# Optimization experiments

Measured on AMD Instinct MI355X. Metric: run time of the kernel, lower is better.

The kernel has to match this reference:

```python
import jax, jax.numpy as jnp
import numpy as np

V, E, H, L, B, S = 32000, 512, 512, 2, 32, 128


def setup_inputs() -> dict:
    key = jax.random.key(0)
    ks = jax.random.split(key, 16)
    sc = 0.05
    return {
        "target": jax.random.randint(ks[0], (B, S), 0, V, dtype=jnp.int32),
        "target_length": jax.random.randint(ks[1], (B,), 1, S, dtype=jnp.int32),
        "context": jax.random.normal(ks[2], (L * 2, B, H), jnp.float32) * 0.1,
        "embed_table": jax.random.normal(ks[3], (V, E), jnp.float32) * sc,
        "w_ih0": jax.random.normal(ks[4], (2, 3 * H, E), jnp.float32) * sc,
        "w_hh0": jax.random.normal(ks[5], (2, 3 * H, H), jnp.float32) * sc,
        "b_ih0": jax.random.normal(ks[6], (2, 3 * H), jnp.float32) * sc,
        "b_hh0": jax.random.normal(ks[7], (2, 3 * H), jnp.float32) * sc,
        "w_ih1": jax.random.normal(ks[8], (2, 3 * H, 2 * H), jnp.float32) * sc,
        "w_hh1": jax.random.normal(ks[9], (2, 3 * H, H), jnp.float32) * sc,
        "b_ih1": jax.random.normal(ks[10], (2, 3 * H), jnp.float32) * sc,
        "b_hh1": jax.random.normal(ks[11], (2, 3 * H), jnp.float32) * sc,
        "fc_w": jax.random.normal(ks[12], (V, 2 * H), jnp.float32) * sc,
        "fc_b": jax.random.normal(ks[13], (V,), jnp.float32) * sc,
    }


def _gru_cell(x, h, w_ih, w_hh, b_ih, b_hh):
    # x: [B, in]  h: [2, B, H]  w_ih: [2, 3H, in]  w_hh: [2, 3H, H]
    gi = jnp.einsum('bi,dgi->dbg', x, w_ih) + b_ih[:, None, :]
    gh = jnp.einsum('dbh,dgh->dbg', h, w_hh) + b_hh[:, None, :]
    ir, iz, in_ = jnp.split(gi, 3, axis=-1)
    hr, hz, hn = jnp.split(gh, 3, axis=-1)
    r = jax.nn.sigmoid(ir + hr)
    z = jax.nn.sigmoid(iz + hz)
    n = jnp.tanh(in_ + r * hn)
    return (1.0 - z) * n + z * h  # [2, B, H]


def reference(target, target_length, context, embed_table,
              w_ih0, w_hh0, b_ih0, b_hh0,
              w_ih1, w_hh1, b_ih1, b_hh1,
              fc_w, fc_b):
    b, s = target.shape
    hd = context.shape[-1]
    emb = embed_table[target]                  # [B, S, E] (dropout = identity in eval)
    h0 = context.reshape(L, 2, b, hd)          # torch layout hidden[l*2+d]
    params = [(w_ih0, w_hh0, b_ih0, b_hh0), (w_ih1, w_hh1, b_ih1, b_hh1)]

    def step(h, x_t):                          # h: [L, 2, B, H], x_t: [B, E]
        x = x_t
        new_h = []
        for l in range(L):
            hn = _gru_cell(x, h[l], *params[l])            # [2, B, H]
            new_h.append(hn)
            x = hn.transpose(1, 0, 2).reshape(b, 2 * hd)   # concat fwd|bwd
        return jnp.stack(new_h), x

    _, outs = jax.lax.scan(step, h0, emb.transpose(1, 0, 2))  # outs: [S, B, 2H]
    out = outs.transpose(1, 0, 2)                              # [B, S, 2H]
    logits = jnp.einsum('bsh,vh->bsv', out, fc_w) + fc_b       # [B, S, V]
    return jax.nn.log_softmax(logits, axis=-1)
```

## Files before the change

### kernel.cpp

```cpp
#include <hip/hip_runtime.h>
#include <cstdint>
#include <cstddef>

#define Vv 32000
#define Ee 512
#define Hh 512
#define Bb 32
#define Ss 128

typedef __bf16 bf16x8 __attribute__((ext_vector_type(8)));
typedef float  f32x4  __attribute__((ext_vector_type(4)));
typedef unsigned long long ull;

__device__ __forceinline__ float b2f(unsigned short u) {
  union { unsigned int i; float f; } v; v.i = ((unsigned int)u) << 16; return v.f;
}
__device__ __forceinline__ unsigned short f2b(float f) {
  union { float f; unsigned int i; } v; v.f = f;
  unsigned int r = v.i + 0x7FFFu + ((v.i >> 16) & 1u);
  return (unsigned short)(r >> 16);
}
__device__ __forceinline__ float sigm(float x) { return 1.f / (1.f + __expf(-x)); }

__device__ __forceinline__ ull aload8(const unsigned short* p) {
  return __hip_atomic_load((const ull*)p, __ATOMIC_RELAXED, __HIP_MEMORY_SCOPE_AGENT);
}
__device__ __forceinline__ void astore8(unsigned short* p, ull v) {
  __hip_atomic_store((ull*)p, v, __ATOMIC_RELAXED, __HIP_MEMORY_SCOPE_AGENT);
}

__device__ __forceinline__ void gl_lds16(const unsigned short* g, unsigned short* l) {
  __builtin_amdgcn_global_load_lds(
      (const __attribute__((address_space(1))) void*)g,
      (__attribute__((address_space(3))) void*)l, 16, 0, 0);
}


__global__ void zero_flags(unsigned* p) {
  for (int i = threadIdx.x; i < 4096; i += 256) p[i] = 0u;
}

__global__ void cast_bf16(const float* __restrict__ src, unsigned short* __restrict__ dst, int n4) {
  int i = blockIdx.x * 256 + threadIdx.x;
  if (i >= n4) return;
  float4 v = reinterpret_cast<const float4*>(src)[i];
  ushort4 o;
  o.x = f2b(v.x); o.y = f2b(v.y); o.z = f2b(v.z); o.w = f2b(v.w);
  reinterpret_cast<ushort4*>(dst)[i] = o;
}

__global__ void pack_w1(const float* __restrict__ ih, const float* __restrict__ hh,
                        unsigned short* __restrict__ dst) {
  int r = blockIdx.x;
  const float* si = ih + (size_t)r * 1024;
  const float* sh = hh + (size_t)r * 512;
  unsigned short* dr = dst + (size_t)r * 1536;
  for (int c = threadIdx.x; c < 1024; c += 256) dr[c] = f2b(si[c]);
  for (int c = threadIdx.x; c < 512; c += 256) dr[1024 + c] = f2b(sh[c]);
}

__global__ void embed_gather(const int* __restrict__ target, const float* __restrict__ table,
                             unsigned short* __restrict__ emb) {
  int sb = blockIdx.x;
  int s = sb >> 5, b = sb & 31;
  int tok = target[b * Ss + s];
  float4 v = reinterpret_cast<const float4*>(table + (size_t)tok * Ee)[threadIdx.x];
  ushort4 o;
  o.x = f2b(v.x); o.y = f2b(v.y); o.z = f2b(v.z); o.w = f2b(v.w);
  reinterpret_cast<ushort4*>(emb + (size_t)sb * Ee)[threadIdx.x] = o;
}

template <int MODE>
__global__ __launch_bounds__(256, 2) void gemm_nt(
    const unsigned short* __restrict__ A, const unsigned short* __restrict__ Bm,
    const float* __restrict__ bias, void* __restrict__ Cout,
    int K, int ldc, size_t sBz, size_t sCz, size_t sBiasz,
    float* __restrict__ pm, float* __restrict__ ps) {
  int z = blockIdx.z;
  Bm += z * sBz;
  bias += z * sBiasz;

  __shared__ __align__(16) unsigned short As[128 * 64];
  __shared__ __align__(16) unsigned short Bs[128 * 64];
  __shared__ float smx[128][2], sse[128][2];

  int t = threadIdx.x;
  int bx, by;
  if (MODE == 1) {
    int lin = blockIdx.x + (int)gridDim.x * blockIdx.y;
    int q = (int)(gridDim.x * gridDim.y) >> 3;
    int wg = (lin & 7) * q + (lin >> 3);
    bx = wg & 31; by = wg >> 5;
  } else {
    bx = blockIdx.x; by = blockIdx.y;
  }
  int m0 = bx * 128, n0 = by * 128;
  int wave = t >> 6, lane = t & 63;
  int wr = wave >> 1, wc = wave & 1;

  f32x4 acc[4][4] = {};

  int kt = K >> 6;
  for (int ks = 0; ks < kt; ++ks) {
    int k0 = ks << 6;
#pragma unroll
    for (int c = 0; c < 4; ++c) {
      int v = c * 256 + t;
      int row = v >> 3, col = (v & 7) * 8;
      int vb = (c * 256 + (t & 192)) * 8;
      gl_lds16(A + (size_t)(m0 + row) * K + k0 + col, As + vb);
      gl_lds16(Bm + (size_t)(n0 + row) * K + k0 + col, Bs + vb);
    }
    __syncthreads();
#pragma unroll
    for (int kk = 0; kk < 2; ++kk) {
      bf16x8 af[4], bfr[4];
      int lrow = lane & 15, lk = kk * 32 + (lane >> 4) * 8;
#pragma unroll
      for (int m = 0; m < 4; ++m)
        af[m] = *reinterpret_cast<const bf16x8*>(As + (wr * 64 + m * 16 + lrow) * 64 + lk);
#pragma unroll
      for (int n = 0; n < 4; ++n)
        bfr[n] = *reinterpret_cast<const bf16x8*>(Bs + (wc * 64 + n * 16 + lrow) * 64 + lk);
#pragma unroll
      for (int m = 0; m < 4; ++m)
#pragma unroll
        for (int n = 0; n < 4; ++n)
          acc[m][n] = __builtin_amdgcn_mfma_f32_16x16x32_bf16(af[m], bfr[n], acc[m][n], 0, 0, 0);
    }
    __syncthreads();
  }

  int lrow4 = (lane >> 4) * 4, lcol = lane & 15;
  if (MODE == 0) {
#pragma unroll
    for (int m = 0; m < 4; ++m) {
      int rbase = m0 + wr * 64 + m * 16 + lrow4;
#pragma unroll
      for (int n = 0; n < 4; ++n) {
        int col = n0 + wc * 64 + n * 16 + lcol;
        float bv = bias[col];
#pragma unroll
        for (int j = 0; j < 4; ++j) {
          int r = rbase + j;
          float vv = acc[m][n][j] + bv;
          ((unsigned short*)Cout)[z * sCz + (size_t)r * ldc + col] = f2b(vv);
        }
      }
    }
  } else {
    float bv[4];
#pragma unroll
    for (int n = 0; n < 4; ++n) bv[n] = bias[n0 + wc * 64 + n * 16 + lcol];
#pragma unroll
    for (int m = 0; m < 4; ++m) {
#pragma unroll
      for (int j = 0; j < 4; ++j) {
        float x[4];
#pragma unroll
        for (int n = 0; n < 4; ++n) x[n] = acc[m][n][j] + bv[n];
        int rib = wr * 64 + m * 16 + lrow4 + j;
        int r = m0 + rib;
        int b = r & 31, s = r >> 5;
        float* crow = (float*)Cout + (size_t)(b * Ss + s) * ldc;
#pragma unroll
        for (int n = 0; n < 4; ++n)
          __builtin_nontemporal_store(x[n], crow + n0 + wc * 64 + n * 16 + lcol);
        float mx = fmaxf(fmaxf(x[0], x[1]), fmaxf(x[2], x[3]));
#pragma unroll
        for (int msk = 1; msk < 16; msk <<= 1) mx = fmaxf(mx, __shfl_xor(mx, msk, 16));
        float se = __expf(x[0] - mx) + __expf(x[1] - mx) + __expf(x[2] - mx) + __expf(x[3] - mx);
#pragma unroll
        for (int msk = 1; msk < 16; msk <<= 1) se += __shfl_xor(se, msk, 16);
        if (lcol == 0) { smx[rib][wc] = mx; sse[rib][wc] = se; }
      }
    }
    __syncthreads();
    if (t < 128) {
      float ma = smx[t][0], mb = smx[t][1];
      float M = fmaxf(ma, mb);
      float S = sse[t][0] * __expf(ma - M) + sse[t][1] * __expf(mb - M);
      int rg = m0 + t;
      int b = rg & 31, s = rg >> 5;
      size_t orow = (size_t)(b * Ss + s);
      pm[orow * 250 + by] = M;
      ps[orow * 250 + by] = S;
    }
  }
}


#define MFMA16 __builtin_amdgcn_mfma_f32_16x16x32_bf16
#define L1_STRIDE 1544
#define L0_STRIDE 520

__global__ __launch_bounds__(384, 1) void pers_kernel(
    const unsigned short* __restrict__ gi0,
    const unsigned short* __restrict__ whh0b, const unsigned short* __restrict__ w1cat,
    const float* __restrict__ b_hh0, const float* __restrict__ b_ih1, const float* __restrict__ b_hh1,
    const float* __restrict__ context,
    unsigned short* __restrict__ XH, unsigned short* __restrict__ H0,
    unsigned short* __restrict__ outs, unsigned* bar) {
  extern __shared__ __align__(16) unsigned short A_lds[];
  __shared__ float pre[7][16][33];
  __shared__ float hf[32][16];
  __shared__ float bA[16], bB[16], bC[16], bD[16];
  __shared__ unsigned sAbort;

  unsigned* flags = bar;
  unsigned* abortf = bar + 3072;

  const int tid = threadIdx.x, blk = blockIdx.x;
  const int w = tid >> 6, lane = tid & 63, ln = lane & 15;
  const int hi8 = (lane >> 4) * 8;
  const bool isL1 = blk < 64;
  const int d = (blk & 63) >> 5, j0 = (blk & 31) * 16;
  const int g = w >> 1, kh = w & 1;

  if (tid == 0) sAbort = 0u;

  auto stile = [&](int s, f32x4 v0, f32x4 v1) {
    int c = ln, r0 = (lane >> 4) * 4;
#pragma unroll
    for (int j = 0; j < 4; ++j) {
      pre[s][c][r0 + j] = v0[j];
      pre[s][c][16 + r0 + j] = v1[j];
    }
  };

  bf16x8 wreg[24];
  if (isL1) {
    const unsigned short* Bw =
        w1cat + ((size_t)d * 1536 + g * 512 + j0 + ln) * 1536 + kh * 768 + hi8;
#pragma unroll
    for (int i = 0; i < 24; ++i) wreg[i] = *reinterpret_cast<const bf16x8*>(Bw + i * 32);
  } else {
    const unsigned short* Bw =
        whh0b + ((size_t)d * 1536 + g * 512 + j0 + ln) * 512 + kh * 256 + hi8;
#pragma unroll
    for (int i = 0; i < 8; ++i) wreg[i] = *reinterpret_cast<const bf16x8*>(Bw + i * 32);
  }

  if (tid < 16) {
    int jj = tid;
    if (isL1) {
      bA[jj] = b_ih1[d * 1536 + j0 + jj] + b_hh1[d * 1536 + j0 + jj];
      bB[jj] = b_ih1[d * 1536 + 512 + j0 + jj] + b_hh1[d * 1536 + 512 + j0 + jj];
      bC[jj] = b_ih1[d * 1536 + 1024 + j0 + jj];
      bD[jj] = b_hh1[d * 1536 + 1024 + j0 + jj];
    } else {
      bA[jj] = b_hh0[d * 1536 + j0 + jj];
      bB[jj] = b_hh0[d * 1536 + 512 + j0 + jj];
      bC[jj] = b_hh0[d * 1536 + 1024 + j0 + jj];
    }
  }
  {
    int layer = isL1 ? 1 : 0;
    for (int i = tid; i < 128; i += 384) {
      int b = i >> 2, j4 = (i & 3) * 4;
      ull pk = 0;
#pragma unroll
      for (int k = 0; k < 4; ++k) {
        float c = context[(((size_t)layer * 2 + d) * 32 + b) * 512 + j0 + j4 + k];
        hf[b][j4 + k] = c;
        pk |= ((ull)f2b(c)) << (16 * k);
      }
      if (isL1) astore8(XH + (size_t)b * 2048 + 1024 + d * 512 + j0 + j4, pk);
      else      astore8(H0 + (size_t)3 * 32768 + ((size_t)d * 32 + b) * 512 + j0 + j4, pk);
    }
  }
  __syncthreads();
  if (tid == 0)
    __hip_atomic_store(flags + (size_t)blk * 16, 1u, __ATOMIC_RELAXED, __HIP_MEMORY_SCOPE_AGENT);

  for (int p = 0; p <= 128; ++p) {
    ull gr = 0, gz2 = 0, gn2 = 0;
    if (!isL1 && p <= 127 && tid < 128) {
      const unsigned short* gzp =
          gi0 + ((size_t)d * 128 + p) * 32 * 1536 + (size_t)(tid >> 2) * 1536 + j0 + (tid & 3) * 4;
      gr  = *(const ull*)(gzp);
      gz2 = *(const ull*)(gzp + 512);
      gn2 = *(const ull*)(gzp + 1024);
    }

    if (w < 2) {
      int idx = -1, tgt = 0;
      if (isL1) {
        if (w == 0) { if (lane < 64) { idx = 64 + lane; tgt = p + 1; } }
        else        { if (lane < 32) { idx = d * 32 + lane; tgt = p + 1; } }
      } else {
        if (w == 0) { if (lane < 32) { idx = 64 + d * 32 + lane; tgt = p + 1; } }
        else        { if (lane < 64) { idx = lane; tgt = p - 1; } }
      }
      ull t0 = __builtin_amdgcn_s_memrealtime();
      while (true) {
        int f = (idx >= 0)
            ? (int)__hip_atomic_load(flags + (size_t)idx * 16, __ATOMIC_RELAXED, __HIP_MEMORY_SCOPE_AGENT)
            : 0x7FFFFFF;
        if (__all(f >= tgt)) break;
        if ((__builtin_amdgcn_s_memrealtime() - t0) > 100000000ULL ||
            __hip_atomic_load(abortf, __ATOMIC_RELAXED, __HIP_MEMORY_SCOPE_AGENT) != 0u) {
          __hip_atomic_store(abortf, 1u, __ATOMIC_RELAXED, __HIP_MEMORY_SCOPE_AGENT);
          sAbort = 1u;
          break;
        }
        __builtin_amdgcn_s_sleep(1);
      }
    }
    __syncthreads();
    if (sAbort) return;

    int rs = (p - 1) & 3, wslot = p & 3;

    if (isL1) {
      if (p >= 1) {
        const unsigned short* XHp = XH + (size_t)rs * 65536;
        int col = tid * 4;
        int gcol = (col < 1024) ? col : (1024 + d * 512 + (col - 1024));
        const unsigned short* src = XHp + gcol;
        unsigned short* dstl = A_lds + col;
        ull v[32];
#pragma unroll
        for (int b = 0; b < 32; ++b) v[b] = aload8(src + (size_t)b * 2048);
#pragma unroll
        for (int b = 0; b < 32; ++b) *(ull*)(dstl + b * L1_STRIDE) = v[b];
      }
    } else {
      if (p <= 127) {
        const unsigned short* H0p = H0 + (size_t)rs * 32768 + (size_t)d * 32 * 512;
        ull v[11];
#pragma unroll
        for (int k = 0; k < 11; ++k) {
          int idx = tid + k * 384;
          if (idx < 4096) v[k] = aload8(H0p + (size_t)(idx >> 7) * 512 + (idx & 127) * 4);
        }
#pragma unroll
        for (int k = 0; k < 11; ++k) {
          int idx = tid + k * 384;
          if (idx < 4096) *(ull*)(A_lds + (idx >> 7) * L0_STRIDE + (idx & 127) * 4) = v[k];
        }
      }
    }
    __syncthreads();

    if (isL1) {
      if (p >= 1) {
        f32x4 p0 = {}, p1 = {}, q0 = {}, q1 = {};
        const unsigned short* al = A_lds + kh * 768 + hi8;
        if (g == 2 && kh == 1) {
#pragma unroll
          for (int i = 0; i < 8; ++i) {
            bf16x8 a0 = *reinterpret_cast<const bf16x8*>(al + ln * L1_STRIDE + i * 32);
            bf16x8 a1 = *reinterpret_cast<const bf16x8*>(al + (ln + 16) * L1_STRIDE + i * 32);
            p0 = MFMA16(a0, wreg[i], p0, 0, 0, 0);
            p1 = MFMA16(a1, wreg[i], p1, 0, 0, 0);
          }
#pragma unroll
          for (int i = 8; i < 24; ++i) {
            bf16x8 a0 = *reinterpret_cast<const bf16x8*>(al + ln * L1_STRIDE + i * 32);
            bf16x8 a1 = *reinterpret_cast<const bf16x8*>(al + (ln + 16) * L1_STRIDE + i * 32);
            q0 = MFMA16(a0, wreg[i], q0, 0, 0, 0);
            q1 = MFMA16(a1, wreg[i], q1, 0, 0, 0);
          }
          stile(5, p0, p1);
          stile(6, q0, q1);
        } else {
#pragma unroll
          for (int i = 0; i < 24; ++i) {
            bf16x8 a0 = *reinterpret_cast<const bf16x8*>(al + ln * L1_STRIDE + i * 32);
            bf16x8 a1 = *reinterpret_cast<const bf16x8*>(al + (ln + 16) * L1_STRIDE + i * 32);
            p0 = MFMA16(a0, wreg[i], p0, 0, 0, 0);
            p1 = MFMA16(a1, wreg[i], p1, 0, 0, 0);
          }
          stile((g < 2) ? g * 2 + kh : 4, p0, p1);
        }
      }
    } else {
      if (p <= 127) {
        f32x4 p0 = {}, p1 = {};
        const unsigned short* al = A_lds + kh * 256 + hi8;
#pragma unroll
        for (int i = 0; i < 8; ++i) {
          bf16x8 a0 = *reinterpret_cast<const bf16x8*>(al + ln * L0_STRIDE + i * 32);
          bf16x8 a1 = *reinterpret_cast<const bf16x8*>(al + (ln + 16) * L0_STRIDE + i * 32);
          p0 = MFMA16(a0, wreg[i], p0, 0, 0, 0);
          p1 = MFMA16(a1, wreg[i], p1, 0, 0, 0);
        }
        stile((g < 2) ? g * 2 + kh : 4 + kh, p0, p1);
      }
    }
    __syncthreads();

    if (isL1) {
      if (p >= 1 && tid < 128) {
        int t_ = p - 1;
        int b = tid >> 2, j4 = (tid & 3) * 4;
        ull pk = 0;
#pragma unroll
        for (int k = 0; k < 4; ++k) {
          int jj = j4 + k;
          float r = sigm(pre[0][jj][b] + pre[1][jj][b] + bA[jj]);
          float z = sigm(pre[2][jj][b] + pre[3][jj][b] + bB[jj]);
          float nn = tanhf(pre[4][jj][b] + pre[5][jj][b] + bC[jj] +
                           r * (pre[6][jj][b] + bD[jj]));
          float h = hf[b][jj];
          float hnew = (1.f - z) * nn + z * h;
          hf[b][jj] = hnew;
          pk |= ((ull)f2b(hnew)) << (16 * k);
        }
        astore8(XH + (size_t)wslot * 65536 + (size_t)b * 2048 + 1024 + d * 512 + j0 + j4, pk);
        __builtin_nontemporal_store(
            pk, (ull*)(outs + ((size_t)t_ * 32 + b) * 1024 + (size_t)d * 512 + j0 + j4));
      }
    } else {
      if (p <= 127 && tid < 128) {
        int b = tid >> 2, j4 = (tid & 3) * 4;
        int col = j0 + j4;
        ull pk = 0;
#pragma unroll
        for (int k = 0; k < 4; ++k) {
          int jj = j4 + k;
          float gir = b2f((unsigned short)(gr >> (16 * k)));
          float giz = b2f((unsigned short)(gz2 >> (16 * k)));
          float gin = b2f((unsigned short)(gn2 >> (16 * k)));
          float r = sigm(gir + pre[0][jj][b] + pre[1][jj][b] + bA[jj]);
          float z = sigm(giz + pre[2][jj][b] + pre[3][jj][b] + bB[jj]);
          float nn = tanhf(gin + r * (pre[4][jj][b] + pre[5][jj][b] + bC[jj]));
          float h = hf[b][jj];
          float hnew = (1.f - z) * nn + z * h;
          hf[b][jj] = hnew;
          pk |= ((ull)f2b(hnew)) << (16 * k);
        }
        astore8(H0 + (size_t)wslot * 32768 + ((size_t)d * 32 + b) * 512 + col, pk);
        astore8(XH + (size_t)wslot * 65536 + (size_t)b * 2048 + d * 512 + col, pk);
      }
    }
    __syncthreads();
    if (tid == 0)
      __hip_atomic_store(flags + (size_t)blk * 16, (unsigned)(p + 2),
                         __ATOMIC_RELAXED, __HIP_MEMORY_SCOPE_AGENT);
    if (!isL1 && p == 127) return;
  }
}


__global__ __launch_bounds__(128) void lse_reduce(const float* __restrict__ pm,
                                                  const float* __restrict__ ps,
                                                  float* __restrict__ lsebuf) {
  int r = blockIdx.x * 128 + threadIdx.x;
  const float* pmr = pm + (size_t)r * 250;
  const float* psr = ps + (size_t)r * 250;
  float M = -1e30f, S = 0.f;
  for (int i = 0; i < 250; ++i) {
    float m2 = pmr[i], s2 = psr[i];
    if (m2 <= M) {
      S += s2 * __expf(m2 - M);
    } else {
      S = S * __expf(M - m2) + s2;
      M = m2;
    }
  }
  lsebuf[r] = M + __logf(S);
}

__global__ __launch_bounds__(256) void sub_lse(float* __restrict__ out,
                                               const float* __restrict__ lsebuf) {
  int row = blockIdx.x;
  float l = lsebuf[row];
  f32x4* rp = (f32x4*)(out + (size_t)row * Vv);
  for (int i = threadIdx.x; i < 8000; i += 256) {
    f32x4 v = __builtin_nontemporal_load(rp + i);
    v[0] -= l; v[1] -= l; v[2] -= l; v[3] -= l;
    __builtin_nontemporal_store(v, rp + i);
  }
}


extern "C" void kernel_launch(void* const* d_in, const int* in_sizes, int n_in,
                              void* d_out, int out_size, void* d_ws, size_t ws_size,
                              hipStream_t stream) {
  (void)in_sizes; (void)n_in; (void)out_size; (void)ws_size;
  const int*   target  = (const int*)  d_in[0];
  const float* context = (const float*)d_in[2];
  const float* table   = (const float*)d_in[3];
  const float* w_ih0   = (const float*)d_in[4];
  const float* w_hh0   = (const float*)d_in[5];
  const float* b_ih0   = (const float*)d_in[6];
  const float* b_hh0   = (const float*)d_in[7];
  const float* w_ih1   = (const float*)d_in[8];
  const float* w_hh1   = (const float*)d_in[9];
  const float* b_ih1   = (const float*)d_in[10];
  const float* b_hh1   = (const float*)d_in[11];
  const float* fc_w    = (const float*)d_in[12];
  const float* fc_b    = (const float*)d_in[13];
  float* out = (float*)d_out;

  uint8_t* ws = (uint8_t*)d_ws;
  size_t off = 0;
  auto alloc = [&](size_t bytes) {
    uint8_t* p = ws + off;
    off += (bytes + 255) & ~(size_t)255;
    return p;
  };
  unsigned*       bar   = (unsigned*)alloc(16384);
  unsigned short* XH    = (unsigned short*)alloc((size_t)4 * 32 * 2048 * 2);
  unsigned short* H0    = (unsigned short*)alloc((size_t)4 * 2 * 32 * 512 * 2);
  unsigned short* whh0b = (unsigned short*)alloc((size_t)1572864 * 2);
  unsigned short* w1cat = (unsigned short*)alloc((size_t)2 * 1536 * 1536 * 2);
  unsigned short* embb  = (unsigned short*)alloc((size_t)2097152 * 2);
  unsigned short* wih0b = (unsigned short*)alloc((size_t)1572864 * 2);
  unsigned short* gi0   = (unsigned short*)alloc((size_t)12582912 * 2);
  unsigned short* outsb = (unsigned short*)alloc((size_t)4194304 * 2);
  unsigned short* fcwb  = (unsigned short*)alloc((size_t)32768000 * 2);

  float* pm     = (float*)gi0;
  float* ps     = pm + (size_t)4096 * 250;
  float* lsebuf = ps + (size_t)4096 * 250;

  static bool attr_done = false;
  if (!attr_done) {
    hipFuncSetAttribute(reinterpret_cast<const void*>(pers_kernel),
                        hipFuncAttributeMaxDynamicSharedMemorySize, 98816);
    attr_done = true;
  }

  zero_flags<<<dim3(1), 256, 0, stream>>>(bar);
  cast_bf16<<<dim3(1536), 256, 0, stream>>>(w_ih0, wih0b, 393216);
  cast_bf16<<<dim3(1536), 256, 0, stream>>>(w_hh0, whh0b, 393216);
  cast_bf16<<<dim3(32000), 256, 0, stream>>>(fc_w, fcwb, 8192000);
  pack_w1<<<dim3(3072), 256, 0, stream>>>(w_ih1, w_hh1, w1cat);
  embed_gather<<<dim3(4096), 128, 0, stream>>>(target, table, embb);

  gemm_nt<0><<<dim3(32, 12, 2), 256, 0, stream>>>(
      embb, wih0b, b_ih0, gi0, 512, 1536,
      (size_t)1536 * 512, (size_t)4096 * 1536, (size_t)1536, nullptr, nullptr);

  pers_kernel<<<dim3(128), 384, 98816, stream>>>(
      gi0, whh0b, w1cat, b_hh0, b_ih1, b_hh1, context, XH, H0, outsb, bar);

  gemm_nt<1><<<dim3(32, 250, 1), 256, 0, stream>>>(
      outsb, fcwb, fc_b, out, 1024, Vv, 0, 0, 0, pm, ps);

  lse_reduce<<<dim3(32), 128, 0, stream>>>(pm, ps, lsebuf);
  sub_lse<<<dim3(4096), 256, 0, stream>>>(out, lsebuf);
}
```

Baseline: 1.356 ms.

## Tag recurrent state with step numbers and overlap fc_w cast with persistent GRU

The persistent GRU kernel now publishes hidden states as 32-bit words that carry a step tag next to each bf16 value. Consumers poll the data itself instead of waiting on per-step flag barriers, the ring buffer grows to 8 slots, and the full flag wait runs only every 4 steps. The fc_w fp32-to-bf16 cast moves into 128 extra blocks of the persistent launch so it runs alongside the serial recurrence, and the small prep kernels are merged into one launch. This cuts per-step synchronisation latency and launch overhead, but doubles the bytes exchanged per step and risks the cast blocks competing with the recurrent blocks for memory bandwidth.

```diff
diff --git a/kernel.cpp b/kernel.cpp
--- a/kernel.cpp
+++ b/kernel.cpp
@@ -22,11 +22,19 @@
 }
 __device__ __forceinline__ float sigm(float x) { return 1.f / (1.f + __expf(-x)); }
 
-__device__ __forceinline__ ull aload8(const unsigned short* p) {
-  return __hip_atomic_load((const ull*)p, __ATOMIC_RELAXED, __HIP_MEMORY_SCOPE_AGENT);
-}
-__device__ __forceinline__ void astore8(unsigned short* p, ull v) {
-  __hip_atomic_store((ull*)p, v, __ATOMIC_RELAXED, __HIP_MEMORY_SCOPE_AGENT);
+__device__ __forceinline__ ull aload8(const ull* p) {
+  return __hip_atomic_load(p, __ATOMIC_RELAXED, __HIP_MEMORY_SCOPE_AGENT);
+}
+__device__ __forceinline__ void astore8(ull* p, ull v) {
+  __hip_atomic_store(p, v, __ATOMIC_RELAXED, __HIP_MEMORY_SCOPE_AGENT);
+}
+__device__ __forceinline__ unsigned pack32(ull v) {
+  return (unsigned)(v & 0xFFFFull) | (unsigned)((v >> 16) & 0xFFFF0000ull);
+}
+__device__ __forceinline__ ull packpair(float a, float b, unsigned tag) {
+  ull lo = (ull)((unsigned)f2b(a) | (tag << 16));
+  ull hi = (ull)((unsigned)f2b(b) | (tag << 16));
+  return lo | (hi << 32);
 }
 
 __device__ __forceinline__ void gl_lds16(const unsigned short* g, unsigned short* l) {
@@ -35,39 +43,42 @@
       (__attribute__((address_space(3))) void*)l, 16, 0, 0);
 }
 
-
-__global__ void zero_flags(unsigned* p) {
-  for (int i = threadIdx.x; i < 4096; i += 256) p[i] = 0u;
-}
-
-__global__ void cast_bf16(const float* __restrict__ src, unsigned short* __restrict__ dst, int n4) {
-  int i = blockIdx.x * 256 + threadIdx.x;
-  if (i >= n4) return;
-  float4 v = reinterpret_cast<const float4*>(src)[i];
-  ushort4 o;
-  o.x = f2b(v.x); o.y = f2b(v.y); o.z = f2b(v.z); o.w = f2b(v.w);
-  reinterpret_cast<ushort4*>(dst)[i] = o;
-}
-
-__global__ void pack_w1(const float* __restrict__ ih, const float* __restrict__ hh,
-                        unsigned short* __restrict__ dst) {
-  int r = blockIdx.x;
-  const float* si = ih + (size_t)r * 1024;
-  const float* sh = hh + (size_t)r * 512;
-  unsigned short* dr = dst + (size_t)r * 1536;
-  for (int c = threadIdx.x; c < 1024; c += 256) dr[c] = f2b(si[c]);
-  for (int c = threadIdx.x; c < 512; c += 256) dr[1024 + c] = f2b(sh[c]);
-}
-
-__global__ void embed_gather(const int* __restrict__ target, const float* __restrict__ table,
-                             unsigned short* __restrict__ emb) {
-  int sb = blockIdx.x;
-  int s = sb >> 5, b = sb & 31;
-  int tok = target[b * Ss + s];
-  float4 v = reinterpret_cast<const float4*>(table + (size_t)tok * Ee)[threadIdx.x];
-  ushort4 o;
-  o.x = f2b(v.x); o.y = f2b(v.y); o.z = f2b(v.z); o.w = f2b(v.w);
-  reinterpret_cast<ushort4*>(emb + (size_t)sb * Ee)[threadIdx.x] = o;
+__global__ __launch_bounds__(256) void prep_all(
+    const float* __restrict__ w_ih0, const float* __restrict__ w_hh0,
+    const float* __restrict__ w_ih1, const float* __restrict__ w_hh1,
+    const int* __restrict__ target, const float* __restrict__ table,
+    unsigned short* __restrict__ wih0b, unsigned short* __restrict__ whh0b,
+    unsigned short* __restrict__ w1cat, unsigned short* __restrict__ emb,
+    unsigned* __restrict__ bar) {
+  int blk = blockIdx.x, t = threadIdx.x;
+  if (blk < 1536) {
+    int i = blk * 256 + t;
+    float4 v = reinterpret_cast<const float4*>(w_ih0)[i];
+    ushort4 o; o.x = f2b(v.x); o.y = f2b(v.y); o.z = f2b(v.z); o.w = f2b(v.w);
+    reinterpret_cast<ushort4*>(wih0b)[i] = o;
+  } else if (blk < 3072) {
+    int i = (blk - 1536) * 256 + t;
+    float4 v = reinterpret_cast<const float4*>(w_hh0)[i];
+    ushort4 o; o.x = f2b(v.x); o.y = f2b(v.y); o.z = f2b(v.z); o.w = f2b(v.w);
+    reinterpret_cast<ushort4*>(whh0b)[i] = o;
+  } else if (blk < 6144) {
+    int r = blk - 3072;
+    const float* si = w_ih1 + (size_t)r * 1024;
+    const float* sh = w_hh1 + (size_t)r * 512;
+    unsigned short* dr = w1cat + (size_t)r * 1536;
+    for (int c = t; c < 1024; c += 256) dr[c] = f2b(si[c]);
+    for (int c = t; c < 512; c += 256) dr[1024 + c] = f2b(sh[c]);
+  } else if (blk < 8192) {
+    int sb = (blk - 6144) * 2 + (t >> 7);
+    int tt = t & 127;
+    int s = sb >> 5, b = sb & 31;
+    int tok = target[b * Ss + s];
+    float4 v = reinterpret_cast<const float4*>(table + (size_t)tok * Ee)[tt];
+    ushort4 o; o.x = f2b(v.x); o.y = f2b(v.y); o.z = f2b(v.z); o.w = f2b(v.w);
+    reinterpret_cast<ushort4*>(emb + (size_t)sb * Ee)[tt] = o;
+  } else {
+    for (int i = t; i < 4096; i += 256) bar[i] = 0u;
+  }
 }
 
 template <int MODE>
@@ -193,14 +204,29 @@
 #define MFMA16 __builtin_amdgcn_mfma_f32_16x16x32_bf16
 #define L1_STRIDE 1544
 #define L0_STRIDE 520
-
-__global__ __launch_bounds__(384, 1) void pers_kernel(
+#define TAGMASK 0xFFFF0000FFFF0000ull
+
+__global__ __launch_bounds__(512, 1) void pers_kernel(
     const unsigned short* __restrict__ gi0,
     const unsigned short* __restrict__ whh0b, const unsigned short* __restrict__ w1cat,
     const float* __restrict__ b_hh0, const float* __restrict__ b_ih1, const float* __restrict__ b_hh1,
     const float* __restrict__ context,
-    unsigned short* __restrict__ XH, unsigned short* __restrict__ H0,
-    unsigned short* __restrict__ outs, unsigned* bar) {
+    unsigned* __restrict__ XO, unsigned* __restrict__ H1,
+    unsigned short* __restrict__ outs, unsigned* bar,
+    const float* __restrict__ fc_w, unsigned short* __restrict__ fcwb) {
+  const int tid = threadIdx.x, blk = blockIdx.x;
+
+  if (blk >= 128) {
+    int base = (blk - 128) * 512 + tid;
+#pragma unroll 5
+    for (int i = base; i < 8192000; i += 65536) {
+      float4 v = reinterpret_cast<const float4*>(fc_w)[i];
+      ushort4 o; o.x = f2b(v.x); o.y = f2b(v.y); o.z = f2b(v.z); o.w = f2b(v.w);
+      reinterpret_cast<ushort4*>(fcwb)[i] = o;
+    }
+    return;
+  }
+
   extern __shared__ __align__(16) unsigned short A_lds[];
   __shared__ float pre[7][16][33];
   __shared__ float hf[32][16];
@@ -210,7 +236,6 @@
   unsigned* flags = bar;
   unsigned* abortf = bar + 3072;
 
-  const int tid = threadIdx.x, blk = blockIdx.x;
   const int w = tid >> 6, lane = tid & 63, ln = lane & 15;
   const int hi8 = (lane >> 4) * 8;
   const bool isL1 = blk < 64;
@@ -219,6 +244,23 @@
 
   if (tid == 0) sAbort = 0u;
 
+  auto pollwait = [&](int idx, unsigned tgt) {
+    ull t0 = __builtin_amdgcn_s_memrealtime();
+    while (true) {
+      unsigned f = (idx >= 0)
+          ? __hip_atomic_load(flags + (size_t)idx * 16, __ATOMIC_RELAXED, __HIP_MEMORY_SCOPE_AGENT)
+          : 0xFFFFFFFu;
+      if (__all(f >= tgt)) break;
+      if ((__builtin_amdgcn_s_memrealtime() - t0) > 100000000ULL ||
+          __hip_atomic_load(abortf, __ATOMIC_RELAXED, __HIP_MEMORY_SCOPE_AGENT) != 0u) {
+        __hip_atomic_store(abortf, 1u, __ATOMIC_RELAXED, __HIP_MEMORY_SCOPE_AGENT);
+        sAbort = 1u;
+        break;
+      }
+      __builtin_amdgcn_s_sleep(1);
+    }
+  };
+
   auto stile = [&](int s, f32x4 v0, f32x4 v1) {
     int c = ln, r0 = (lane >> 4) * 4;
 #pragma unroll
@@ -229,16 +271,18 @@
   };
 
   bf16x8 wreg[24];
-  if (isL1) {
-    const unsigned short* Bw =
-        w1cat + ((size_t)d * 1536 + g * 512 + j0 + ln) * 1536 + kh * 768 + hi8;
-#pragma unroll
-    for (int i = 0; i < 24; ++i) wreg[i] = *reinterpret_cast<const bf16x8*>(Bw + i * 32);
-  } else {
-    const unsigned short* Bw =
-        whh0b + ((size_t)d * 1536 + g * 512 + j0 + ln) * 512 + kh * 256 + hi8;
-#pragma unroll
-    for (int i = 0; i < 8; ++i) wreg[i] = *reinterpret_cast<const bf16x8*>(Bw + i * 32);
+  if (w < 6) {
+    if (isL1) {
+      const unsigned short* Bw =
+          w1cat + ((size_t)d * 1536 + g * 512 + j0 + ln) * 1536 + kh * 768 + hi8;
+#pragma unroll
+      for (int i = 0; i < 24; ++i) wreg[i] = *reinterpret_cast<const bf16x8*>(Bw + i * 32);
+    } else {
+      const unsigned short* Bw =
+          whh0b + ((size_t)d * 1536 + g * 512 + j0 + ln) * 512 + kh * 256 + hi8;
+#pragma unroll
+      for (int i = 0; i < 8; ++i) wreg[i] = *reinterpret_cast<const bf16x8*>(Bw + i * 32);
+    }
   }
 
   if (tid < 16) {
@@ -254,148 +298,214 @@
       bC[jj] = b_hh0[d * 1536 + 1024 + j0 + jj];
     }
   }
-  {
+
+  if (tid < 128) {
+    int b = tid >> 2, j4 = (tid & 3) * 4;
     int layer = isL1 ? 1 : 0;
-    for (int i = tid; i < 128; i += 384) {
-      int b = i >> 2, j4 = (i & 3) * 4;
-      ull pk = 0;
-#pragma unroll
-      for (int k = 0; k < 4; ++k) {
-        float c = context[(((size_t)layer * 2 + d) * 32 + b) * 512 + j0 + j4 + k];
-        hf[b][j4 + k] = c;
-        pk |= ((ull)f2b(c)) << (16 * k);
-      }
-      if (isL1) astore8(XH + (size_t)b * 2048 + 1024 + d * 512 + j0 + j4, pk);
-      else      astore8(H0 + (size_t)3 * 32768 + ((size_t)d * 32 + b) * 512 + j0 + j4, pk);
+    float c0 = context[(((size_t)layer * 2 + d) * 32 + b) * 512 + j0 + j4 + 0];
+    float c1 = context[(((size_t)layer * 2 + d) * 32 + b) * 512 + j0 + j4 + 1];
+    float c2 = context[(((size_t)layer * 2 + d) * 32 + b) * 512 + j0 + j4 + 2];
+    float c3 = context[(((size_t)layer * 2 + d) * 32 + b) * 512 + j0 + j4 + 3];
+    hf[b][j4 + 0] = c0; hf[b][j4 + 1] = c1; hf[b][j4 + 2] = c2; hf[b][j4 + 3] = c3;
+    if (isL1) {
+      ull* dst = (ull*)H1 + ((size_t)(0 * 2 + d) * 32 + b) * 256 + ((j0 + j4) >> 1);
+      astore8(dst, packpair(c0, c1, 1u));
+      astore8(dst + 1, packpair(c2, c3, 1u));
+    } else {
+      ull* dst = (ull*)XO + ((size_t)(7 * 32 + b)) * 512 + d * 256 + ((j0 + j4) >> 1);
+      astore8(dst, packpair(c0, c1, 0u));
+      astore8(dst + 1, packpair(c2, c3, 0u));
+    }
+#pragma unroll
+    for (int s = 0; s < 8; ++s) {
+      if (isL1 ? (s == 0) : (s == 7)) continue;
+      ull* dst = isL1
+          ? (ull*)H1 + (((size_t)s * 2 + d) * 32 + b) * 256 + ((j0 + j4) >> 1)
+          : (ull*)XO + ((size_t)s * 32 + b) * 512 + d * 256 + ((j0 + j4) >> 1);
+      astore8(dst, ~0ull);
+      astore8(dst + 1, ~0ull);
     }
   }
   __syncthreads();
   if (tid == 0)
     __hip_atomic_store(flags + (size_t)blk * 16, 1u, __ATOMIC_RELAXED, __HIP_MEMORY_SCOPE_AGENT);
-
-  for (int p = 0; p <= 128; ++p) {
-    ull gr = 0, gz2 = 0, gn2 = 0;
-    if (!isL1 && p <= 127 && tid < 128) {
-      const unsigned short* gzp =
-          gi0 + ((size_t)d * 128 + p) * 32 * 1536 + (size_t)(tid >> 2) * 1536 + j0 + (tid & 3) * 4;
-      gr  = *(const ull*)(gzp);
-      gz2 = *(const ull*)(gzp + 512);
-      gn2 = *(const ull*)(gzp + 1024);
-    }
-
-    if (w < 2) {
-      int idx = -1, tgt = 0;
-      if (isL1) {
-        if (w == 0) { if (lane < 64) { idx = 64 + lane; tgt = p + 1; } }
-        else        { if (lane < 32) { idx = d * 32 + lane; tgt = p + 1; } }
-      } else {
-        if (w == 0) { if (lane < 32) { idx = 64 + d * 32 + lane; tgt = p + 1; } }
-        else        { if (lane < 64) { idx = lane; tgt = p - 1; } }
-      }
-      ull t0 = __builtin_amdgcn_s_memrealtime();
-      while (true) {
-        int f = (idx >= 0)
-            ? (int)__hip_atomic_load(flags + (size_t)idx * 16, __ATOMIC_RELAXED, __HIP_MEMORY_SCOPE_AGENT)
-            : 0x7FFFFFF;
-        if (__all(f >= tgt)) break;
-        if ((__builtin_amdgcn_s_memrealtime() - t0) > 100000000ULL ||
-            __hip_atomic_load(abortf, __ATOMIC_RELAXED, __HIP_MEMORY_SCOPE_AGENT) != 0u) {
-          __hip_atomic_store(abortf, 1u, __ATOMIC_RELAXED, __HIP_MEMORY_SCOPE_AGENT);
-          sAbort = 1u;
-          break;
-        }
-        __builtin_amdgcn_s_sleep(1);
-      }
-    }
-    __syncthreads();
-    if (sAbort) return;
-
-    int rs = (p - 1) & 3, wslot = p & 3;
-
-    if (isL1) {
-      if (p >= 1) {
-        const unsigned short* XHp = XH + (size_t)rs * 65536;
-        int col = tid * 4;
-        int gcol = (col < 1024) ? col : (1024 + d * 512 + (col - 1024));
-        const unsigned short* src = XHp + gcol;
-        unsigned short* dstl = A_lds + col;
-        ull v[32];
-#pragma unroll
-        for (int b = 0; b < 32; ++b) v[b] = aload8(src + (size_t)b * 2048);
-#pragma unroll
-        for (int b = 0; b < 32; ++b) *(ull*)(dstl + b * L1_STRIDE) = v[b];
-      }
-    } else {
-      if (p <= 127) {
-        const unsigned short* H0p = H0 + (size_t)rs * 32768 + (size_t)d * 32 * 512;
-        ull v[11];
-#pragma unroll
-        for (int k = 0; k < 11; ++k) {
-          int idx = tid + k * 384;
-          if (idx < 4096) v[k] = aload8(H0p + (size_t)(idx >> 7) * 512 + (idx & 127) * 4);
-        }
-#pragma unroll
-        for (int k = 0; k < 11; ++k) {
-          int idx = tid + k * 384;
-          if (idx < 4096) *(ull*)(A_lds + (idx >> 7) * L0_STRIDE + (idx & 127) * 4) = v[k];
-        }
-      }
-    }
-    __syncthreads();
-
-    if (isL1) {
-      if (p >= 1) {
-        f32x4 p0 = {}, p1 = {}, q0 = {}, q1 = {};
-        const unsigned short* al = A_lds + kh * 768 + hi8;
-        if (g == 2 && kh == 1) {
+  if (w == 6) pollwait(lane, 1u);
+  else if (w == 7) pollwait(64 + lane, 1u);
+  __syncthreads();
+  bool dead = (sAbort != 0u);
+
+  if (!dead) {
+    for (int p = 0; p <= 128; ++p) {
+      bool l0act = (!isL1) && p <= 127;
+      bool l1act = isL1 && p >= 1;
+      int s_rd = (p - 1) & 7, s_wr = p & 7;
+      ull ex = ((ull)(unsigned)p << 16) | ((ull)(unsigned)p << 48);
+
+      ull gr = 0, gz2 = 0, gn2 = 0;
+      if (l0act && tid < 128) {
+        const unsigned short* gzp =
+            gi0 + ((size_t)d * 128 + p) * 32 * 1536 + (size_t)(tid >> 2) * 1536 + j0 + (tid & 3) * 4;
+        gr  = *(const ull*)(gzp);
+        gz2 = *(const ull*)(gzp + 512);
+        gn2 = *(const ull*)(gzp + 1024);
+      }
+
+      if ((p & 3) == 0 && p >= 4) {
+        if (isL1) {
+          if (w == 6) pollwait(lane < 32 ? d * 32 + lane : -1, (unsigned)(p - 2));
+        } else if (p <= 127) {
+          if (w == 6) pollwait(lane, (unsigned)(p - 2));
+          else if (w == 7) pollwait(lane < 32 ? 64 + d * 32 + lane : -1, (unsigned)(p - 2));
+        }
+      }
+
+      if (l1act) {
+        const ull* xw = (const ull*)XO + (size_t)s_rd * 16384;
+        const ull* hw = (const ull*)H1 + ((size_t)s_rd * 2 + d) * 8192;
+        ull vx[32], vh[16];
+#pragma unroll
+        for (int k = 0; k < 32; ++k) vx[k] = aload8(xw + tid + k * 512);
+#pragma unroll
+        for (int k = 0; k < 16; ++k) vh[k] = aload8(hw + tid + k * 512);
+        unsigned pendA = 0, pendB = 0;
+#pragma unroll
+        for (int k = 0; k < 32; ++k) {
+          int idx = tid + k * 512, b = idx >> 9, c2 = idx & 511;
+          if (((vx[k] ^ ex) & TAGMASK) == 0)
+            *(unsigned*)(A_lds + (size_t)b * L1_STRIDE + 2 * c2) = pack32(vx[k]);
+          else pendA |= 1u << k;
+        }
+#pragma unroll
+        for (int k = 0; k < 16; ++k) {
+          int idx = tid + k * 512, b = idx >> 8, c2 = idx & 255;
+          if (((vh[k] ^ ex) & TAGMASK) == 0)
+            *(unsigned*)(A_lds + (size_t)b * L1_STRIDE + 1024 + 2 * c2) = pack32(vh[k]);
+          else pendB |= 1u << k;
+        }
+        if (pendA | pendB) {
+          ull t0 = __builtin_amdgcn_s_memrealtime();
+          while (pendA | pendB) {
+#pragma unroll
+            for (int k = 0; k < 32; ++k) if ((pendA >> k) & 1) {
+              ull v = aload8(xw + tid + k * 512);
+              if (((v ^ ex) & TAGMASK) == 0) {
+                int idx = tid + k * 512, b = idx >> 9, c2 = idx & 511;
+                *(unsigned*)(A_lds + (size_t)b * L1_STRIDE + 2 * c2) = pack32(v);
+                pendA &= ~(1u << k);
+              }
+            }
+#pragma unroll
+            for (int k = 0; k < 16; ++k) if ((pendB >> k) & 1) {
+              ull v = aload8(hw + tid + k * 512);
+              if (((v ^ ex) & TAGMASK) == 0) {
+                int idx = tid + k * 512, b = idx >> 8, c2 = idx & 255;
+                *(unsigned*)(A_lds + (size_t)b * L1_STRIDE + 1024 + 2 * c2) = pack32(v);
+                pendB &= ~(1u << k);
+              }
+            }
+            if ((__builtin_amdgcn_s_memrealtime() - t0) > 100000000ULL ||
+                __hip_atomic_load(abortf, __ATOMIC_RELAXED, __HIP_MEMORY_SCOPE_AGENT) != 0u) {
+              __hip_atomic_store(abortf, 1u, __ATOMIC_RELAXED, __HIP_MEMORY_SCOPE_AGENT);
+              sAbort = 1u;
+              break;
+            }
+          }
+        }
+      } else if (l0act) {
+        const ull* xw = (const ull*)XO + (size_t)s_rd * 16384 + d * 256;
+        ull vx[16];
+#pragma unroll
+        for (int k = 0; k < 16; ++k) {
+          int idx = tid + k * 512;
+          vx[k] = aload8(xw + ((size_t)(idx >> 8) << 9) + (idx & 255));
+        }
+        unsigned pendA = 0;
+#pragma unroll
+        for (int k = 0; k < 16; ++k) {
+          int idx = tid + k * 512, b = idx >> 8, c2 = idx & 255;
+          if (((vx[k] ^ ex) & TAGMASK) == 0)
+            *(unsigned*)(A_lds + (size_t)b * L0_STRIDE + 2 * c2) = pack32(vx[k]);
+          else pendA |= 1u << k;
+        }
+        if (pendA) {
+          ull t0 = __builtin_amdgcn_s_memrealtime();
+          while (pendA) {
+#pragma unroll
+            for (int k = 0; k < 16; ++k) if ((pendA >> k) & 1) {
+              int idx = tid + k * 512;
+              ull v = aload8(xw + ((size_t)(idx >> 8) << 9) + (idx & 255));
+              if (((v ^ ex) & TAGMASK) == 0) {
+                int b = idx >> 8, c2 = idx & 255;
+                *(unsigned*)(A_lds + (size_t)b * L0_STRIDE + 2 * c2) = pack32(v);
+                pendA &= ~(1u << k);
+              }
+            }
+            if ((__builtin_amdgcn_s_memrealtime() - t0) > 100000000ULL ||
+                __hip_atomic_load(abortf, __ATOMIC_RELAXED, __HIP_MEMORY_SCOPE_AGENT) != 0u) {
+              __hip_atomic_store(abortf, 1u, __ATOMIC_RELAXED, __HIP_MEMORY_SCOPE_AGENT);
+              sAbort = 1u;
+              break;
+            }
+          }
+        }
+      }
+      __syncthreads();
+      if (sAbort) { dead = true; break; }
+      if (tid == 0 && (l1act || l0act))
+        __hip_atomic_store(flags + (size_t)blk * 16, (unsigned)(p + 2),
+                           __ATOMIC_RELAXED, __HIP_MEMORY_SCOPE_AGENT);
+
+      if (w < 6) {
+        if (l1act) {
+          f32x4 p0 = {}, p1 = {}, q0 = {}, q1 = {};
+          const unsigned short* al = A_lds + kh * 768 + hi8;
+          if (g == 2 && kh == 1) {
+#pragma unroll
+            for (int i = 0; i < 8; ++i) {
+              bf16x8 a0 = *reinterpret_cast<const bf16x8*>(al + ln * L1_STRIDE + i * 32);
+              bf16x8 a1 = *reinterpret_cast<const bf16x8*>(al + (ln + 16) * L1_STRIDE + i * 32);
+              p0 = MFMA16(a0, wreg[i], p0, 0, 0, 0);
+              p1 = MFMA16(a1, wreg[i], p1, 0, 0, 0);
+            }
+#pragma unroll
+            for (int i = 8; i < 24; ++i) {
+              bf16x8 a0 = *reinterpret_cast<const bf16x8*>(al + ln * L1_STRIDE + i * 32);
+              bf16x8 a1 = *reinterpret_cast<const bf16x8*>(al + (ln + 16) * L1_STRIDE + i * 32);
+              q0 = MFMA16(a0, wreg[i], q0, 0, 0, 0);
+              q1 = MFMA16(a1, wreg[i], q1, 0, 0, 0);
+            }
+            stile(5, p0, p1);
+            stile(6, q0, q1);
+          } else {
+#pragma unroll
+            for (int i = 0; i < 24; ++i) {
+              bf16x8 a0 = *reinterpret_cast<const bf16x8*>(al + ln * L1_STRIDE + i * 32);
+              bf16x8 a1 = *reinterpret_cast<const bf16x8*>(al + (ln + 16) * L1_STRIDE + i * 32);
+              p0 = MFMA16(a0, wreg[i], p0, 0, 0, 0);
+              p1 = MFMA16(a1, wreg[i], p1, 0, 0, 0);
+            }
+            stile((g < 2) ? g * 2 + kh : 4, p0, p1);
+          }
+        } else if (l0act) {
+          f32x4 p0 = {}, p1 = {};
+          const unsigned short* al = A_lds + kh * 256 + hi8;
 #pragma unroll
           for (int i = 0; i < 8; ++i) {
-            bf16x8 a0 = *reinterpret_cast<const bf16x8*>(al + ln * L1_STRIDE + i * 32);
-            bf16x8 a1 = *reinterpret_cast<const bf16x8*>(al + (ln + 16) * L1_STRIDE + i * 32);
+            bf16x8 a0 = *reinterpret_cast<const bf16x8*>(al + ln * L0_STRIDE + i * 32);
+            bf16x8 a1 = *reinterpret_cast<const bf16x8*>(al + (ln + 16) * L0_STRIDE + i * 32);
             p0 = MFMA16(a0, wreg[i], p0, 0, 0, 0);
             p1 = MFMA16(a1, wreg[i], p1, 0, 0, 0);
           }
-#pragma unroll
-          for (int i = 8; i < 24; ++i) {
-            bf16x8 a0 = *reinterpret_cast<const bf16x8*>(al + ln * L1_STRIDE + i * 32);
-            bf16x8 a1 = *reinterpret_cast<const bf16x8*>(al + (ln + 16) * L1_STRIDE + i * 32);
-            q0 = MFMA16(a0, wreg[i], q0, 0, 0, 0);
-            q1 = MFMA16(a1, wreg[i], q1, 0, 0, 0);
-          }
-          stile(5, p0, p1);
-          stile(6, q0, q1);
-        } else {
-#pragma unroll
-          for (int i = 0; i < 24; ++i) {
-            bf16x8 a0 = *reinterpret_cast<const bf16x8*>(al + ln * L1_STRIDE + i * 32);
-            bf16x8 a1 = *reinterpret_cast<const bf16x8*>(al + (ln + 16) * L1_STRIDE + i * 32);
-            p0 = MFMA16(a0, wreg[i], p0, 0, 0, 0);
-            p1 = MFMA16(a1, wreg[i], p1, 0, 0, 0);
-          }
-          stile((g < 2) ? g * 2 + kh : 4, p0, p1);
-        }
-      }
-    } else {
-      if (p <= 127) {
-        f32x4 p0 = {}, p1 = {};
-        const unsigned short* al = A_lds + kh * 256 + hi8;
-#pragma unroll
-        for (int i = 0; i < 8; ++i) {
-          bf16x8 a0 = *reinterpret_cast<const bf16x8*>(al + ln * L0_STRIDE + i * 32);
-          bf16x8 a1 = *reinterpret_cast<const bf16x8*>(al + (ln + 16) * L0_STRIDE + i * 32);
-          p0 = MFMA16(a0, wreg[i], p0, 0, 0, 0);
-          p1 = MFMA16(a1, wreg[i], p1, 0, 0, 0);
-        }
-        stile((g < 2) ? g * 2 + kh : 4 + kh, p0, p1);
-      }
-    }
-    __syncthreads();
-
-    if (isL1) {
-      if (p >= 1 && tid < 128) {
+          stile((g < 2) ? g * 2 + kh : 4 + kh, p0, p1);
+        }
+      }
+      __syncthreads();
+
+      unsigned tag = (unsigned)(p + 1);
+      if (l1act && tid < 128) {
         int t_ = p - 1;
         int b = tid >> 2, j4 = (tid & 3) * 4;
-        ull pk = 0;
+        float hn[4];
 #pragma unroll
         for (int k = 0; k < 4; ++k) {
           int jj = j4 + k;
@@ -406,17 +516,18 @@
           float h = hf[b][jj];
           float hnew = (1.f - z) * nn + z * h;
           hf[b][jj] = hnew;
-          pk |= ((ull)f2b(hnew)) << (16 * k);
-        }
-        astore8(XH + (size_t)wslot * 65536 + (size_t)b * 2048 + 1024 + d * 512 + j0 + j4, pk);
+          hn[k] = hnew;
+        }
+        ull* dH = (ull*)H1 + (((size_t)s_wr * 2 + d) * 32 + b) * 256 + ((j0 + j4) >> 1);
+        astore8(dH, packpair(hn[0], hn[1], tag));
+        astore8(dH + 1, packpair(hn[2], hn[3], tag));
+        ull pk = (ull)f2b(hn[0]) | ((ull)f2b(hn[1]) << 16) |
+                 ((ull)f2b(hn[2]) << 32) | ((ull)f2b(hn[3]) << 48);
         __builtin_nontemporal_store(
-            pk, (ull*)(outs + ((size_t)t_ * 32 + b) * 1024 + (size_t)d * 512 + j0 + j4));
-      }
-    } else {
-      if (p <= 127 && tid < 128) {
+            pk, (ull*)(outs + ((size_t)t_ * 32 + b) * 1024 + d * 512 + j0 + j4));
+      } else if (l0act && tid < 128) {
         int b = tid >> 2, j4 = (tid & 3) * 4;
-        int col = j0 + j4;
-        ull pk = 0;
+        float hn[4];
 #pragma unroll
         for (int k = 0; k < 4; ++k) {
           int jj = j4 + k;
@@ -429,17 +540,34 @@
           float h = hf[b][jj];
           float hnew = (1.f - z) * nn + z * h;
           hf[b][jj] = hnew;
-          pk |= ((ull)f2b(hnew)) << (16 * k);
-        }
-        astore8(H0 + (size_t)wslot * 32768 + ((size_t)d * 32 + b) * 512 + col, pk);
-        astore8(XH + (size_t)wslot * 65536 + (size_t)b * 2048 + d * 512 + col, pk);
-      }
+          hn[k] = hnew;
+        }
+        ull* dX = (ull*)XO + ((size_t)s_wr * 32 + b) * 512 + d * 256 + ((j0 + j4) >> 1);
+        astore8(dX, packpair(hn[0], hn[1], tag));
+        astore8(dX + 1, packpair(hn[2], hn[3], tag));
+      }
+    }
+  }
+
+  if (!dead) {
+    if (isL1) {
+      if (w == 6) pollwait(lane < 32 ? d * 32 + lane : -1, 130u);
+    } else {
+      if (w == 6) pollwait(lane, 130u);
+      else if (w == 7) pollwait(lane < 32 ? 64 + d * 32 + lane : -1, 129u);
     }
     __syncthreads();
-    if (tid == 0)
-      __hip_atomic_store(flags + (size_t)blk * 16, (unsigned)(p + 2),
-                         __ATOMIC_RELAXED, __HIP_MEMORY_SCOPE_AGENT);
-    if (!isL1 && p == 127) return;
+  }
+  if (tid < 128) {
+    int b = tid >> 2, j4 = (tid & 3) * 4;
+#pragma unroll
+    for (int s = 0; s < 8; ++s) {
+      ull* dst = isL1
+          ? (ull*)H1 + (((size_t)s * 2 + d) * 32 + b) * 256 + ((j0 + j4) >> 1)
+          : (ull*)XO + ((size_t)s * 32 + b) * 512 + d * 256 + ((j0 + j4) >> 1);
+      astore8(dst, ~0ull);
+      astore8(dst + 1, ~0ull);
+    }
   }
 }
 
@@ -503,8 +631,8 @@
     return p;
   };
   unsigned*       bar   = (unsigned*)alloc(16384);
-  unsigned short* XH    = (unsigned short*)alloc((size_t)4 * 32 * 2048 * 2);
-  unsigned short* H0    = (unsigned short*)alloc((size_t)4 * 2 * 32 * 512 * 2);
+  unsigned*       XO    = (unsigned*)alloc((size_t)8 * 32 * 1024 * 4);
+  unsigned*       H1    = (unsigned*)alloc((size_t)8 * 2 * 32 * 512 * 4);
   unsigned short* whh0b = (unsigned short*)alloc((size_t)1572864 * 2);
   unsigned short* w1cat = (unsigned short*)alloc((size_t)2 * 1536 * 1536 * 2);
   unsigned short* embb  = (unsigned short*)alloc((size_t)2097152 * 2);
@@ -524,19 +652,15 @@
     attr_done = true;
   }
 
-  zero_flags<<<dim3(1), 256, 0, stream>>>(bar);
-  cast_bf16<<<dim3(1536), 256, 0, stream>>>(w_ih0, wih0b, 393216);
-  cast_bf16<<<dim3(1536), 256, 0, stream>>>(w_hh0, whh0b, 393216);
-  cast_bf16<<<dim3(32000), 256, 0, stream>>>(fc_w, fcwb, 8192000);
-  pack_w1<<<dim3(3072), 256, 0, stream>>>(w_ih1, w_hh1, w1cat);
-  embed_gather<<<dim3(4096), 128, 0, stream>>>(target, table, embb);
+  prep_all<<<dim3(8193), 256, 0, stream>>>(w_ih0, w_hh0, w_ih1, w_hh1, target, table,
+                                           wih0b, whh0b, w1cat, embb, bar);
 
   gemm_nt<0><<<dim3(32, 12, 2), 256, 0, stream>>>(
       embb, wih0b, b_ih0, gi0, 512, 1536,
       (size_t)1536 * 512, (size_t)4096 * 1536, (size_t)1536, nullptr, nullptr);
 
-  pers_kernel<<<dim3(128), 384, 98816, stream>>>(
-      gi0, whh0b, w1cat, b_hh0, b_ih1, b_hh1, context, XH, H0, outsb, bar);
+  pers_kernel<<<dim3(256), 512, 98816, stream>>>(
+      gi0, whh0b, w1cat, b_hh0, b_ih1, b_hh1, context, XO, H1, outsb, bar, fc_w, fcwb);
 
   gemm_nt<1><<<dim3(32, 250, 1), 256, 0, stream>>>(
       outsb, fcwb, fc_b, out, 1024, Vv, 0, 0, 0, pm, ps);
```

Result: slower. 2.119 ms (+56.2%).
